# Optimization experiments

Measured on AMD Instinct MI355X. Metric: run time of the kernel, lower is better.

The kernel has to match this reference:

```python
import jax, jax.numpy as jnp
import numpy as np

B_SZ, L, H, P, G, N, CS = 2, 2048, 32, 64, 1, 128, 256


def _i8(k, shape):
    return jax.random.randint(k, shape, -127, 128, dtype=jnp.int32).astype(jnp.int8)


def setup_inputs() -> dict:
    key = jax.random.key(0)
    k = jax.random.split(key, 7)
    return {
        "x": _i8(k[0], (B_SZ, L, H, P)),          # quantized int8 activations
        "dt": _i8(k[1], (B_SZ, L, H)),
        "B": _i8(k[2], (B_SZ, L, G, N)),
        "C": _i8(k[3], (B_SZ, L, G, N)),
        "q_A_log": _i8(k[4], (H,)),               # int8 quantized A_log
        "q_D": _i8(k[5], (H,)),                   # int8 quantized D (D_has_hdim=False)
        "dt_bias": jax.random.normal(k[6], (H,), jnp.float32) * 0.1,
        "A_log_scale": jnp.float32(0.02),
        "D_scale": jnp.float32(0.01),
        "dt_scale": jnp.float32(0.03),
        "x_scale": jnp.float32(0.05),
        "B_scale": jnp.float32(0.05),
        "C_scale": jnp.float32(0.05),
    }


def _chunk_scan(x, dt, B, C, q_A_log, q_D, dt_bias,
                A_log_scale, D_scale, dt_scale, x_scale, B_scale, C_scale):
    f32 = jnp.float32
    b, l, h, p = x.shape
    g, n = B.shape[2], B.shape[3]
    cs = CS
    nc = l // cs

    # --- inline dequantization (per-tensor scales, nhead/ndim groups == 0) ---
    xf = x.astype(f32) * x_scale                       # (b, l, h, p)
    dtf = jax.nn.softplus(dt.astype(f32) * dt_scale + dt_bias)   # (b, l, h), dt_limit=(0, inf)
    A = -jnp.exp(q_A_log.astype(f32) * A_log_scale)    # (h,)
    Bf = B.astype(f32) * B_scale                       # (b, l, g, n)
    Cf = C.astype(f32) * C_scale

    # --- chunk the sequence ---
    xc = xf.reshape(b, nc, cs, h, p)
    dtc = dtf.reshape(b, nc, cs, h)
    Bc = Bf.reshape(b, nc, cs, g, n)
    Cc = Cf.reshape(b, nc, cs, g, n)
    rep = h // g
    Bh = jnp.repeat(Bc, rep, axis=3)                   # (b, nc, cs, h, n)
    Ch = jnp.repeat(Cc, rep, axis=3)

    dA = dtc * A                                       # (b, nc, cs, h), <= 0
    cum = jnp.cumsum(dA, axis=2)                       # cumulative log-decay within chunk

    # --- per-chunk states: sum_s exp(cum[-1]-cum[s]) * dt[s] * B[s] (x) x[s] ---
    decay_states = jnp.exp(cum[:, :, -1:, :] - cum)    # (b, nc, cs, h)
    states = jnp.einsum('bzlhn,bzlh,bzlhp->bzhpn', Bh, dtc * decay_states, xc)

    # --- inter-chunk recurrence (sequential scan over chunks) ---
    chunk_decay = jnp.exp(cum[:, :, -1, :])            # (b, nc, h)

    def step(carry, inp):
        s_c, d_c = inp                                 # (b, h, p, n), (b, h)
        new = d_c[:, :, None, None] * carry + s_c
        return new, carry                              # emit state entering this chunk

    states_t = jnp.moveaxis(states, 1, 0)              # (nc, b, h, p, n)
    decay_t = jnp.moveaxis(chunk_decay, 1, 0)          # (nc, b, h)
    final_state, prev_states = jax.lax.scan(
        step, jnp.zeros((b, h, p, n), f32), (states_t, decay_t))
    prev_states = jnp.moveaxis(prev_states, 0, 1)      # (b, nc, h, p, n)

    # --- inter-chunk output: C[l] . state_in * exp(cum[l]) ---
    y_inter = jnp.einsum('bzlhn,bzhpn,bzlh->bzlhp', Ch, prev_states, jnp.exp(cum))

    # --- intra-chunk output: causal (C.B) attention with decay weights ---
    cumT = jnp.moveaxis(cum, 3, 2)                     # (b, nc, h, cs)
    diff = cumT[..., :, None] - cumT[..., None, :]     # (b, nc, h, cs, cs): cum[l]-cum[s]
    mask = jnp.tril(jnp.ones((cs, cs), bool))
    decay_m = jnp.exp(jnp.where(mask, diff, -jnp.inf)) # zero above diagonal, no overflow
    scores = (jnp.einsum('bzlhn,bzshn->bzhls', Ch, Bh)
              * decay_m
              * jnp.moveaxis(dtc, 3, 2)[..., None, :])
    y_intra = jnp.einsum('bzhls,bzshp->bzlhp', scores, xc)

    # --- skip connection D * x (per-head D) ---
    Df = q_D.astype(f32) * D_scale                     # (h,)
    y = (y_intra + y_inter).reshape(b, l, h, p) + xf * Df[None, None, :, None]
    return y


def reference(x, dt, B, C, q_A_log, q_D, dt_bias,
              A_log_scale, D_scale, dt_scale, x_scale, B_scale, C_scale):
    return _chunk_scan(x, dt, B, C, q_A_log, q_D, dt_bias,
                       A_log_scale, D_scale, dt_scale, x_scale, B_scale, C_scale)
```

## Files before the change

kernel.cpp:

```cpp
#include <hip/hip_runtime.h>
#include <math.h>

#define BB 2
#define LSEQ 2048
#define H 32
#define PDIM 64
#define NDIM 128
#define CS 256
#define NC 8

typedef _Float16 half8 __attribute__((ext_vector_type(8)));
typedef _Float16 half4 __attribute__((ext_vector_type(4)));
typedef float floatx4 __attribute__((ext_vector_type(4)));


__device__ __forceinline__ int dot4i8(int a, int b, int c) {
#if __has_builtin(__builtin_amdgcn_sdot4)
    return __builtin_amdgcn_sdot4(a, b, c, false);
#else
    c += ((a << 24) >> 24) * ((b << 24) >> 24);
    c += ((a << 16) >> 24) * ((b << 16) >> 24);
    c += ((a << 8) >> 24) * ((b << 8) >> 24);
    c += (a >> 24) * (b >> 24);
    return c;
#endif
}

__global__ __launch_bounds__(256) void kA(
    const int* __restrict__ Bm, const int* __restrict__ Cm,
    const float* __restrict__ Bs_p, const float* __restrict__ Cs_p,
    _Float16* __restrict__ CBh, _Float16* __restrict__ Bt16T, _Float16* __restrict__ C16T)
{
    __shared__ int Bi[64][33];
    __shared__ int Ci[64][33];
    int t = threadIdx.x;
    int r = blockIdx.x % 26;
    int zz = blockIdx.x / 26;
    int z = zz & 7, b = zz >> 3;
    int bz = b * NC + z;
    if (r < 10) {
        const int LT[10] = {0,1,1,2,2,2,3,3,3,3};
        const int ST[10] = {0,0,1,0,1,2,0,1,2,3};
        int l0 = LT[r] * 64, s0 = ST[r] * 64;
        const int* Bp = Bm + (size_t)(b * LSEQ + z * CS + s0) * NDIM;
        const int* Cp = Cm + (size_t)(b * LSEQ + z * CS + l0) * NDIM;
        for (int i = t; i < 64 * 32; i += 256) {
            int rr = i >> 5, k = i & 31;
            const int* sb = Bp + rr * NDIM + k * 4;
            const int* sc = Cp + rr * NDIM + k * 4;
            Bi[rr][k] = (sb[0] & 255) | ((sb[1] & 255) << 8) | ((sb[2] & 255) << 16) | ((sb[3] & 255) << 24);
            Ci[rr][k] = (sc[0] & 255) | ((sc[1] & 255) << 8) | ((sc[2] & 255) << 16) | ((sc[3] & 255) << 24);
        }
        __syncthreads();
        float cbscale = (*Bs_p) * (*Cs_p);
        int ll = t & 63, lg = t >> 6;
        int acc[16];
#pragma unroll
        for (int i = 0; i < 16; ++i) acc[i] = 0;
        for (int k = 0; k < 32; ++k) {
            int cw = Ci[ll][k];
#pragma unroll
            for (int si = 0; si < 16; ++si)
                acc[si] = dot4i8(cw, Bi[lg * 16 + si][k], acc[si]);
        }
        int l = l0 + ll;
        int l16 = l >> 4, lm = l & 15;
        int sb8 = (s0 + lg * 16) >> 3;
        _Float16* bp = CBh + ((size_t)(bz * 16 + l16) * 32 + sb8) * 128 + lm * 8;
#pragma unroll
        for (int g = 0; g < 2; ++g) {
            half8 v;
#pragma unroll
            for (int i = 0; i < 8; ++i) v[i] = (_Float16)((float)acc[g * 8 + i] * cbscale);
            *(half8*)(bp + g * 128) = v;
        }
    } else {
        int slice = r - 10;
        {
            int lm = t >> 4, n8 = t & 15;
            const int* cp = Cm + (size_t)(b * LSEQ + z * CS + slice * 16 + lm) * NDIM + n8 * 8;
            int4 c0 = *(const int4*)cp;
            int4 c1 = *(const int4*)(cp + 4);
            half8 v;
            v[0] = (_Float16)(float)c0.x; v[1] = (_Float16)(float)c0.y;
            v[2] = (_Float16)(float)c0.z; v[3] = (_Float16)(float)c0.w;
            v[4] = (_Float16)(float)c1.x; v[5] = (_Float16)(float)c1.y;
            v[6] = (_Float16)(float)c1.z; v[7] = (_Float16)(float)c1.w;
            *(half8*)(C16T + ((size_t)(bz * 16 + slice) * 16 + n8) * 128 + lm * 8) = v;
        }
        {
            int nm = t & 15, s8l = t >> 4;
            int n16 = slice & 7, s8 = (slice >> 3) * 16 + s8l;
            const int* bp = Bm + (size_t)(b * LSEQ + z * CS + s8 * 8) * NDIM + n16 * 16 + nm;
            half8 v;
#pragma unroll
            for (int j = 0; j < 8; ++j) v[j] = (_Float16)(float)bp[(size_t)j * NDIM];
            *(half8*)(Bt16T + ((size_t)(bz * 8 + n16) * 32 + s8) * 128 + nm * 8) = v;
        }
    }
}

#define P16_STRIDE 4360
__global__ __launch_bounds__(256) void k013(
    const int* __restrict__ dt, const int* __restrict__ qA, const float* __restrict__ dt_bias,
    const float* __restrict__ A_scale_p, const float* __restrict__ dt_scale_p,
    const int* __restrict__ xq, const float* __restrict__ xs_p, const float* __restrict__ Bs_p,
    const _Float16* __restrict__ Bt16T,
    float* __restrict__ cum, float* __restrict__ cAg, float* __restrict__ cdecay,
    signed char* __restrict__ x8, _Float16* __restrict__ statesF16)
{
    __shared__ float cumS[CS];
    __shared__ float cB[CS];
    __shared__ float wsum[4];
    __shared__ _Float16 xcS[3 * P16_STRIDE + 31 * 136 + 128];
    int t = threadIdx.x;
    int h = blockIdx.x & 31, z = (blockIdx.x >> 5) & 7, b = blockIdx.x >> 8;
    int bz = b * NC + z, bzh = bz * H + h;
    int lane6 = t & 63, w = t >> 6;

    float A = -__expf((float)qA[h] * (*A_scale_p));
    float raw = (float)dt[(size_t)(b * LSEQ + z * CS + t) * H + h];
    float xin = raw * (*dt_scale_p) + dt_bias[h];
    float sp = (xin > 20.f) ? xin : log1pf(__expf(xin));
    float v = sp * A;
#pragma unroll
    for (int off = 1; off < 64; off <<= 1) {
        float u = __shfl_up(v, off, 64);
        if (lane6 >= off) v += u;
    }
    if (lane6 == 63) wsum[w] = v;
    __syncthreads();
    float add = 0.f;
    for (int wv = 0; wv < w; ++wv) add += wsum[wv];
    float cumv = v + add;
    float cl = wsum[0] + wsum[1] + wsum[2] + wsum[3];
    float xs = *xs_p;
    cum[(size_t)bzh * CS + t] = cumv;
    cAg[(size_t)bzh * CS + t] = sp * xs;
    if (t == 0) cdecay[bzh] = __expf(cl);
    cumS[t] = cumv;
    cB[t] = sp * __expf(cl - cumv) * xs * (*Bs_p);
    __syncthreads();

    int pq = t & 15, srow = t >> 4;
    const int* xb = xq + ((size_t)(b * LSEQ + z * CS) * H + h) * PDIM + pq * 4;
    signed char* x8b = x8 + ((size_t)(b * LSEQ + z * CS) * H + h) * PDIM + pq * 4;
    int p0 = pq * 4;
    int pbase = (p0 >> 4) * P16_STRIDE + ((p0 & 15) * 8);
    for (int j = 0; j < 16; ++j) {
        int s = j * 16 + srow;
        int4 w4 = *(const int4*)(xb + (size_t)s * (H * PDIM));
        float c = cB[s];
        int sbase = pbase + (s >> 3) * 136 + (s & 7);
        signed char pk[4];
        int xi[4] = {w4.x, w4.y, w4.z, w4.w};
#pragma unroll
        for (int pp = 0; pp < 4; ++pp) {
            xcS[sbase + pp * 8] = (_Float16)((float)xi[pp] * c);
            pk[pp] = (signed char)xi[pp];
        }
        *(int*)(x8b + (size_t)s * (H * PDIM)) = *(int*)pk;
    }
    __syncthreads();

    int m = lane6 & 15, q = lane6 >> 4;
    const _Float16* abase = xcS + w * P16_STRIDE + m * 8;
    const _Float16* bbase = Bt16T + (size_t)(bz * 8) * 32 * 128 + m * 8;
    floatx4 acc[8] = {};
    for (int kk = 0; kk < 8; ++kk) {
        if (cl - cumS[kk * 32 + 31] < -30.f) continue;
        int s8k = kk * 4 + q;
        half8 a = *(const half8*)(abase + s8k * 136);
#pragma unroll
        for (int nt = 0; nt < 8; ++nt) {
            half8 bf = *(const half8*)(bbase + ((size_t)nt * 32 + s8k) * 128);
            acc[nt] = __builtin_amdgcn_mfma_f32_16x16x32_f16(a, bf, acc[nt], 0, 0, 0);
        }
    }
    _Float16* sb = statesF16 + (size_t)bzh * 8192;
#pragma unroll
    for (int nt = 0; nt < 8; ++nt)
#pragma unroll
        for (int rr = 0; rr < 4; ++rr)
            sb[(size_t)(w * 16 + nt * 2 + (m >> 3)) * 128 + (q * 4 + rr) * 8 + (m & 7)] =
                (_Float16)(acc[nt][rr] * 0.0625f);
}

__global__ __launch_bounds__(256) void k4_scan(
    const float* __restrict__ cdecay, const _Float16* __restrict__ statesF16,
    _Float16* __restrict__ statesHT)
{
    int idx = blockIdx.x * 256 + threadIdx.x;
    int off4 = (idx & 2047) * 4;
    int h = (idx >> 11) & 31, b = idx >> 16;
    floatx4 carry = {};
    for (int z = 0; z < NC; ++z) {
        int bzh = (b * NC + z) * H + h;
        half4 v4 = *(const half4*)(statesF16 + (size_t)bzh * 8192 + off4);
        float d = cdecay[bzh];
        half4 o;
#pragma unroll
        for (int i = 0; i < 4; ++i) o[i] = (_Float16)carry[i];
        *(half4*)(statesHT + (size_t)bzh * 8192 + off4) = o;
#pragma unroll
        for (int i = 0; i < 4; ++i) carry[i] = d * carry[i] + (float)v4[i];
    }
}

#define XT_PITCH 136
__global__ __launch_bounds__(256) void k56(
    const signed char* __restrict__ x8, const int* __restrict__ qD,
    const float* __restrict__ cum, const float* __restrict__ cAg,
    const _Float16* __restrict__ CBh, const _Float16* __restrict__ C16T,
    const _Float16* __restrict__ statesHT,
    const float* __restrict__ Cs_p, const float* __restrict__ xs_p, const float* __restrict__ Ds_p,
    float* __restrict__ out)
{
    __shared__ float cumL[CS];
    __shared__ __align__(16) char smem[4 * 32 * XT_PITCH * 2];
    _Float16* xT = (_Float16*)smem;
    float (*ep)[65] = (float(*)[65])smem;
    int t = threadIdx.x;
    int h = blockIdx.x & 31, z = (blockIdx.x >> 5) & 7, b = blockIdx.x >> 8;
    int bz = b * NC + z, bzh = bz * H + h;
    cumL[t] = cum[(size_t)bzh * CS + t];
    float cav = cAg[(size_t)bzh * CS + t];

    {
        const signed char* xrow = x8 + ((size_t)(b * LSEQ + z * CS + t) * H + h) * PDIM;
        int s8 = t >> 3, sj = t & 7;
        int4 r4 = *(const int4*)xrow;
        int4 r5 = *(const int4*)(xrow + 16);
        int4 r6 = *(const int4*)(xrow + 32);
        int4 r7 = *(const int4*)(xrow + 48);
        int words[16] = {r4.x, r4.y, r4.z, r4.w, r5.x, r5.y, r5.z, r5.w,
                         r6.x, r6.y, r6.z, r6.w, r7.x, r7.y, r7.z, r7.w};
#pragma unroll
        for (int wi = 0; wi < 16; ++wi) {
            int wv = words[wi];
#pragma unroll
            for (int bi = 0; bi < 4; ++bi) {
                int p = wi * 4 + bi;
                int val = (wv << (24 - 8 * bi)) >> 24;
                xT[((p >> 4) * 32 + s8) * XT_PITCH + (p & 15) * 8 + sj] =
                    (_Float16)((float)val * cav);
            }
        }
    }
    __syncthreads();

    int w = t >> 6, lane = t & 63, m = lane & 15, q = lane >> 4;
    floatx4 acc[4][4] = {};

    const _Float16* shb = statesHT + (size_t)bzh * 8192 + m * 8;
    const _Float16* cbase = C16T + (size_t)bz * 16 * 16 * 128 + m * 8;
    bool interact[4];
#pragma unroll
    for (int j = 0; j < 4; ++j) interact[j] = (cumL[(4 * j + w) * 16] > -80.f);
    for (int kk = 0; kk < 4; ++kk) {
        int n8 = kk * 4 + q;
        half8 bf[4];
#pragma unroll
        for (int pt = 0; pt < 4; ++pt)
            bf[pt] = *(const half8*)(shb + (pt * 16 + n8) * 128);
#pragma unroll
        for (int j = 0; j < 4; ++j) {
            if (!interact[j]) continue;
            half8 ha = *(const half8*)(cbase + ((size_t)(4 * j + w) * 16 + n8) * 128);
#pragma unroll
            for (int pt = 0; pt < 4; ++pt)
                acc[j][pt] = __builtin_amdgcn_mfma_f32_16x16x32_f16(ha, bf[pt], acc[j][pt], 0, 0, 0);
        }
    }
    float Cs16 = (*Cs_p) * 16.0f;
#pragma unroll
    for (int j = 0; j < 4; ++j)
#pragma unroll
        for (int r = 0; r < 4; ++r) {
            float e = __expf(cumL[(4 * j + w) * 16 + q * 4 + r]) * Cs16;
#pragma unroll
            for (int pt = 0; pt < 4; ++pt) acc[j][pt][r] *= e;
        }

    const _Float16* cbtb = CBh + (size_t)bz * 16 * 32 * 128 + m * 8;
    for (int kk = 0; kk < 8; ++kk) {
        int jmin = (2 * kk - w + 3) >> 2;
        if (jmin < 0) jmin = 0;
        if (jmin > 3) continue;
        int s8 = kk * 4 + q;
        half8 bf[4];
#pragma unroll
        for (int pt = 0; pt < 4; ++pt)
            bf[pt] = *(const half8*)(xT + (size_t)(pt * 32 + s8) * XT_PITCH + m * 8);
#pragma unroll
        for (int j = 0; j < 4; ++j) {
            if (j < jmin) continue;
            int l16 = 4 * j + w;
            if (cumL[l16 * 16] - cumL[kk * 32 + 31] < -30.f) continue;
            int lA = l16 * 16 + m;
            float cum_l = cumL[lA];
            half8 cb8 = *(const half8*)(cbtb + ((size_t)l16 * 32 + s8) * 128);
            half8 a;
#pragma unroll
            for (int jj = 0; jj < 8; ++jj) {
                int s = kk * 32 + q * 8 + jj;
                float wv = (float)cb8[jj] * __expf(cum_l - cumL[s]);
                a[jj] = (_Float16)((s <= lA) ? wv : 0.f);
            }
#pragma unroll
            for (int pt = 0; pt < 4; ++pt)
                acc[j][pt] = __builtin_amdgcn_mfma_f32_16x16x32_f16(a, bf[pt], acc[j][pt], 0, 0, 0);
        }
    }

    float xsDf = (*xs_p) * ((float)qD[h] * (*Ds_p));
    __syncthreads();
#pragma unroll
    for (int pass = 0; pass < 2; ++pass) {
#pragma unroll
        for (int jj = 0; jj < 2; ++jj) {
            int j = pass * 2 + jj;
            int lbase = (((4 * j + w) * 16) & 127) + q * 4;
#pragma unroll
            for (int r = 0; r < 4; ++r)
#pragma unroll
                for (int pt = 0; pt < 4; ++pt)
                    ep[lbase + r][pt * 16 + m] = acc[j][pt][r];
        }
        __syncthreads();
        int lloc = t >> 1;
        int l = pass * 128 + lloc;
        size_t go = ((size_t)(b * LSEQ + z * CS + l) * H + h) * PDIM + (t & 1) * 32;
        const float* er = &ep[lloc][(t & 1) * 32];
        const signed char* xp8 = x8 + go;
#pragma unroll
        for (int it = 0; it < 8; ++it) {
            int xw = *(const int*)(xp8 + it * 4);
            floatx4 vv;
            vv[0] = er[it * 4 + 0] + (float)((xw << 24) >> 24) * xsDf;
            vv[1] = er[it * 4 + 1] + (float)((xw << 16) >> 24) * xsDf;
            vv[2] = er[it * 4 + 2] + (float)((xw << 8) >> 24) * xsDf;
            vv[3] = er[it * 4 + 3] + (float)(xw >> 24) * xsDf;
            *(floatx4*)(out + go + it * 4) = vv;
        }
        __syncthreads();
    }
}

extern "C" void kernel_launch(void* const* d_in, const int* in_sizes, int n_in,
                              void* d_out, int out_size, void* d_ws, size_t ws_size,
                              hipStream_t stream)
{
    const int* xq = (const int*)d_in[0];
    const int* dt = (const int*)d_in[1];
    const int* Bm = (const int*)d_in[2];
    const int* Cm = (const int*)d_in[3];
    const int* qA = (const int*)d_in[4];
    const int* qD = (const int*)d_in[5];
    const float* dt_bias = (const float*)d_in[6];
    const float* A_scale = (const float*)d_in[7];
    const float* D_scale = (const float*)d_in[8];
    const float* dt_scale = (const float*)d_in[9];
    const float* x_scale = (const float*)d_in[10];
    const float* B_scale = (const float*)d_in[11];
    const float* C_scale = (const float*)d_in[12];
    float* out = (float*)d_out;

    char* ws = (char*)d_ws;
    float* cum           = (float*)(ws);
    float* cAg           = (float*)(ws + 524288);
    float* cdecay        = (float*)(ws + 1048576);
    _Float16* CBh        = (_Float16*)(ws + 1050624);
    _Float16* statesF16  = (_Float16*)(ws + 3147776);
    _Float16* statesHT   = (_Float16*)(ws + 11536384);
    _Float16* Bt16T      = (_Float16*)(ws + 19924992);
    _Float16* C16T       = (_Float16*)(ws + 20973568);
    signed char* x8      = (signed char*)(ws + 22022144);

    kA<<<dim3(416), dim3(256), 0, stream>>>(Bm, Cm, B_scale, C_scale, CBh, Bt16T, C16T);
    k013<<<dim3(512), dim3(256), 0, stream>>>(dt, qA, dt_bias, A_scale, dt_scale,
                                              xq, x_scale, B_scale, Bt16T,
                                              cum, cAg, cdecay, x8, statesF16);
    k4_scan<<<dim3(512), dim3(256), 0, stream>>>(cdecay, statesF16, statesHT);
    k56<<<dim3(512), dim3(256), 0, stream>>>(x8, qD, cum, cAg, CBh, C16T, statesHT,
                                             C_scale, x_scale, D_scale, out);
}
```

Before: 157.4 us.

## Split state and output kernels across two blocks per chunk-head for more parallelism

k013 and k56 now launch 1024 blocks instead of 512. Each chunk-head pair is split in two: by P-dimension halves in the state kernel and by interleaved L-row groups in the output kernel. Per-block LDS and accumulators shrink, and launch bounds request 4 blocks per SM, which should raise occupancy on the 256-CU device. The cost is duplicated cumsum/softplus work and duplicated xT staging in both halves. A small cumL vector-load change in the intra-chunk loop is also included.

```diff
diff --git a/kernel.cpp b/kernel.cpp
--- a/kernel.cpp
+++ b/kernel.cpp
@@ -101,7 +101,7 @@
 }
 
 #define P16_STRIDE 4360
-__global__ __launch_bounds__(256) void k013(
+__global__ __launch_bounds__(256, 4) void k013(
     const int* __restrict__ dt, const int* __restrict__ qA, const float* __restrict__ dt_bias,
     const float* __restrict__ A_scale_p, const float* __restrict__ dt_scale_p,
     const int* __restrict__ xq, const float* __restrict__ xs_p, const float* __restrict__ Bs_p,
@@ -112,9 +112,11 @@
     __shared__ float cumS[CS];
     __shared__ float cB[CS];
     __shared__ float wsum[4];
-    __shared__ _Float16 xcS[3 * P16_STRIDE + 31 * 136 + 128];
+    __shared__ _Float16 xcS[P16_STRIDE + 31 * 136 + 136];
     int t = threadIdx.x;
-    int h = blockIdx.x & 31, z = (blockIdx.x >> 5) & 7, b = blockIdx.x >> 8;
+    int half = blockIdx.x & 1;
+    int id = blockIdx.x >> 1;
+    int h = id & 31, z = (id >> 5) & 7, b = id >> 8;
     int bz = b * NC + z, bzh = bz * H + h;
     int lane6 = t & 63, w = t >> 6;
 
@@ -135,20 +137,23 @@
     float cumv = v + add;
     float cl = wsum[0] + wsum[1] + wsum[2] + wsum[3];
     float xs = *xs_p;
-    cum[(size_t)bzh * CS + t] = cumv;
-    cAg[(size_t)bzh * CS + t] = sp * xs;
-    if (t == 0) cdecay[bzh] = __expf(cl);
+    if (half == 0) {
+        cum[(size_t)bzh * CS + t] = cumv;
+        cAg[(size_t)bzh * CS + t] = sp * xs;
+        if (t == 0) cdecay[bzh] = __expf(cl);
+    }
     cumS[t] = cumv;
     cB[t] = sp * __expf(cl - cumv) * xs * (*Bs_p);
     __syncthreads();
 
-    int pq = t & 15, srow = t >> 4;
-    const int* xb = xq + ((size_t)(b * LSEQ + z * CS) * H + h) * PDIM + pq * 4;
-    signed char* x8b = x8 + ((size_t)(b * LSEQ + z * CS) * H + h) * PDIM + pq * 4;
-    int p0 = pq * 4;
-    int pbase = (p0 >> 4) * P16_STRIDE + ((p0 & 15) * 8);
-    for (int j = 0; j < 16; ++j) {
-        int s = j * 16 + srow;
+    int pq = t & 7, srow = t >> 3;
+    int p0 = half * 32 + pq * 4;
+    const int* xb = xq + ((size_t)(b * LSEQ + z * CS) * H + h) * PDIM + p0;
+    signed char* x8b = x8 + ((size_t)(b * LSEQ + z * CS) * H + h) * PDIM + p0;
+    int plocal = pq * 4;
+    int pbase = (plocal >> 4) * P16_STRIDE + ((plocal & 15) * 8);
+    for (int j = 0; j < 8; ++j) {
+        int s = j * 32 + srow;
         int4 w4 = *(const int4*)(xb + (size_t)s * (H * PDIM));
         float c = cB[s];
         int sbase = pbase + (s >> 3) * 136 + (s & 7);
@@ -164,25 +169,27 @@
     __syncthreads();
 
     int m = lane6 & 15, q = lane6 >> 4;
-    const _Float16* abase = xcS + w * P16_STRIDE + m * 8;
+    int p16l = w & 1, ntb = (w >> 1) * 4;
+    const _Float16* abase = xcS + p16l * P16_STRIDE + m * 8;
     const _Float16* bbase = Bt16T + (size_t)(bz * 8) * 32 * 128 + m * 8;
-    floatx4 acc[8] = {};
+    floatx4 acc[4] = {};
     for (int kk = 0; kk < 8; ++kk) {
         if (cl - cumS[kk * 32 + 31] < -30.f) continue;
         int s8k = kk * 4 + q;
         half8 a = *(const half8*)(abase + s8k * 136);
 #pragma unroll
-        for (int nt = 0; nt < 8; ++nt) {
-            half8 bf = *(const half8*)(bbase + ((size_t)nt * 32 + s8k) * 128);
+        for (int nt = 0; nt < 4; ++nt) {
+            half8 bf = *(const half8*)(bbase + ((size_t)(ntb + nt) * 32 + s8k) * 128);
             acc[nt] = __builtin_amdgcn_mfma_f32_16x16x32_f16(a, bf, acc[nt], 0, 0, 0);
         }
     }
+    int p16g = half * 2 + p16l;
     _Float16* sb = statesF16 + (size_t)bzh * 8192;
 #pragma unroll
-    for (int nt = 0; nt < 8; ++nt)
+    for (int nt = 0; nt < 4; ++nt)
 #pragma unroll
         for (int rr = 0; rr < 4; ++rr)
-            sb[(size_t)(w * 16 + nt * 2 + (m >> 3)) * 128 + (q * 4 + rr) * 8 + (m & 7)] =
+            sb[(size_t)(p16g * 16 + (ntb + nt) * 2 + (m >> 3)) * 128 + (q * 4 + rr) * 8 + (m & 7)] =
                 (_Float16)(acc[nt][rr] * 0.0625f);
 }
 
@@ -208,7 +215,7 @@
 }
 
 #define XT_PITCH 136
-__global__ __launch_bounds__(256) void k56(
+__global__ __launch_bounds__(256, 4) void k56(
     const signed char* __restrict__ x8, const int* __restrict__ qD,
     const float* __restrict__ cum, const float* __restrict__ cAg,
     const _Float16* __restrict__ CBh, const _Float16* __restrict__ C16T,
@@ -221,7 +228,9 @@
     _Float16* xT = (_Float16*)smem;
     float (*ep)[65] = (float(*)[65])smem;
     int t = threadIdx.x;
-    int h = blockIdx.x & 31, z = (blockIdx.x >> 5) & 7, b = blockIdx.x >> 8;
+    int par = blockIdx.x & 1;
+    int id = blockIdx.x >> 1;
+    int h = id & 31, z = (id >> 5) & 7, b = id >> 8;
     int bz = b * NC + z, bzh = bz * H + h;
     cumL[t] = cum[(size_t)bzh * CS + t];
     float cav = cAg[(size_t)bzh * CS + t];
@@ -250,13 +259,13 @@
     __syncthreads();
 
     int w = t >> 6, lane = t & 63, m = lane & 15, q = lane >> 4;
-    floatx4 acc[4][4] = {};
+    floatx4 acc[2][4] = {};
 
     const _Float16* shb = statesHT + (size_t)bzh * 8192 + m * 8;
     const _Float16* cbase = C16T + (size_t)bz * 16 * 16 * 128 + m * 8;
-    bool interact[4];
-#pragma unroll
-    for (int j = 0; j < 4; ++j) interact[j] = (cumL[(4 * j + w) * 16] > -80.f);
+    bool interact[2];
+#pragma unroll
+    for (int jl = 0; jl < 2; ++jl) interact[jl] = (cumL[(4 * par + 8 * jl + w) * 16] > -80.f);
     for (int kk = 0; kk < 4; ++kk) {
         int n8 = kk * 4 + q;
         half8 bf[4];
@@ -264,38 +273,40 @@
         for (int pt = 0; pt < 4; ++pt)
             bf[pt] = *(const half8*)(shb + (pt * 16 + n8) * 128);
 #pragma unroll
-        for (int j = 0; j < 4; ++j) {
-            if (!interact[j]) continue;
-            half8 ha = *(const half8*)(cbase + ((size_t)(4 * j + w) * 16 + n8) * 128);
+        for (int jl = 0; jl < 2; ++jl) {
+            if (!interact[jl]) continue;
+            int l16 = 4 * par + 8 * jl + w;
+            half8 ha = *(const half8*)(cbase + ((size_t)l16 * 16 + n8) * 128);
 #pragma unroll
             for (int pt = 0; pt < 4; ++pt)
-                acc[j][pt] = __builtin_amdgcn_mfma_f32_16x16x32_f16(ha, bf[pt], acc[j][pt], 0, 0, 0);
+                acc[jl][pt] = __builtin_amdgcn_mfma_f32_16x16x32_f16(ha, bf[pt], acc[jl][pt], 0, 0, 0);
         }
     }
     float Cs16 = (*Cs_p) * 16.0f;
 #pragma unroll
-    for (int j = 0; j < 4; ++j)
+    for (int jl = 0; jl < 2; ++jl)
 #pragma unroll
         for (int r = 0; r < 4; ++r) {
-            float e = __expf(cumL[(4 * j + w) * 16 + q * 4 + r]) * Cs16;
-#pragma unroll
-            for (int pt = 0; pt < 4; ++pt) acc[j][pt][r] *= e;
+            float e = __expf(cumL[(4 * par + 8 * jl + w) * 16 + q * 4 + r]) * Cs16;
+#pragma unroll
+            for (int pt = 0; pt < 4; ++pt) acc[jl][pt][r] *= e;
         }
 
     const _Float16* cbtb = CBh + (size_t)bz * 16 * 32 * 128 + m * 8;
+    int l16max = 4 * par + 8 + w;
     for (int kk = 0; kk < 8; ++kk) {
-        int jmin = (2 * kk - w + 3) >> 2;
-        if (jmin < 0) jmin = 0;
-        if (jmin > 3) continue;
+        if (l16max < 2 * kk) continue;
         int s8 = kk * 4 + q;
         half8 bf[4];
 #pragma unroll
         for (int pt = 0; pt < 4; ++pt)
             bf[pt] = *(const half8*)(xT + (size_t)(pt * 32 + s8) * XT_PITCH + m * 8);
-#pragma unroll
-        for (int j = 0; j < 4; ++j) {
-            if (j < jmin) continue;
-            int l16 = 4 * j + w;
+        floatx4 c0 = *(const floatx4*)(&cumL[kk * 32 + q * 8]);
+        floatx4 c1 = *(const floatx4*)(&cumL[kk * 32 + q * 8 + 4]);
+#pragma unroll
+        for (int jl = 0; jl < 2; ++jl) {
+            int l16 = 4 * par + 8 * jl + w;
+            if (l16 < 2 * kk) continue;
             if (cumL[l16 * 16] - cumL[kk * 32 + 31] < -30.f) continue;
             int lA = l16 * 16 + m;
             float cum_l = cumL[lA];
@@ -304,32 +315,32 @@
 #pragma unroll
             for (int jj = 0; jj < 8; ++jj) {
                 int s = kk * 32 + q * 8 + jj;
-                float wv = (float)cb8[jj] * __expf(cum_l - cumL[s]);
+                float cls = (jj < 4) ? c0[jj] : c1[jj - 4];
+                float wv = (float)cb8[jj] * __expf(cum_l - cls);
                 a[jj] = (_Float16)((s <= lA) ? wv : 0.f);
             }
 #pragma unroll
             for (int pt = 0; pt < 4; ++pt)
-                acc[j][pt] = __builtin_amdgcn_mfma_f32_16x16x32_f16(a, bf[pt], acc[j][pt], 0, 0, 0);
+                acc[jl][pt] = __builtin_amdgcn_mfma_f32_16x16x32_f16(a, bf[pt], acc[jl][pt], 0, 0, 0);
         }
     }
 
     float xsDf = (*xs_p) * ((float)qD[h] * (*Ds_p));
     __syncthreads();
 #pragma unroll
-    for (int pass = 0; pass < 2; ++pass) {
-#pragma unroll
-        for (int jj = 0; jj < 2; ++jj) {
-            int j = pass * 2 + jj;
-            int lbase = (((4 * j + w) * 16) & 127) + q * 4;
-#pragma unroll
-            for (int r = 0; r < 4; ++r)
-#pragma unroll
-                for (int pt = 0; pt < 4; ++pt)
-                    ep[lbase + r][pt * 16 + m] = acc[j][pt][r];
-        }
-        __syncthreads();
+    for (int jl = 0; jl < 2; ++jl) {
+        int lbase = jl * 64 + w * 16 + q * 4;
+#pragma unroll
+        for (int r = 0; r < 4; ++r)
+#pragma unroll
+            for (int pt = 0; pt < 4; ++pt)
+                ep[lbase + r][pt * 16 + m] = acc[jl][pt][r];
+    }
+    __syncthreads();
+    {
         int lloc = t >> 1;
-        int l = pass * 128 + lloc;
+        int jl = lloc >> 6, wv = (lloc >> 4) & 3, lm = lloc & 15;
+        int l = (4 * par + 8 * jl + wv) * 16 + lm;
         size_t go = ((size_t)(b * LSEQ + z * CS + l) * H + h) * PDIM + (t & 1) * 32;
         const float* er = &ep[lloc][(t & 1) * 32];
         const signed char* xp8 = x8 + go;
@@ -343,7 +354,6 @@
             vv[3] = er[it * 4 + 3] + (float)(xw >> 24) * xsDf;
             *(floatx4*)(out + go + it * 4) = vv;
         }
-        __syncthreads();
     }
 }
 
@@ -378,10 +388,10 @@
     signed char* x8      = (signed char*)(ws + 22022144);
 
     kA<<<dim3(416), dim3(256), 0, stream>>>(Bm, Cm, B_scale, C_scale, CBh, Bt16T, C16T);
-    k013<<<dim3(512), dim3(256), 0, stream>>>(dt, qA, dt_bias, A_scale, dt_scale,
-                                              xq, x_scale, B_scale, Bt16T,
-                                              cum, cAg, cdecay, x8, statesF16);
+    k013<<<dim3(1024), dim3(256), 0, stream>>>(dt, qA, dt_bias, A_scale, dt_scale,
+                                               xq, x_scale, B_scale, Bt16T,
+                                               cum, cAg, cdecay, x8, statesF16);
     k4_scan<<<dim3(512), dim3(256), 0, stream>>>(cdecay, statesF16, statesHT);
-    k56<<<dim3(512), dim3(256), 0, stream>>>(x8, qD, cum, cAg, CBh, C16T, statesHT,
-                                             C_scale, x_scale, D_scale, out);
-}
+    k56<<<dim3(1024), dim3(256), 0, stream>>>(x8, qD, cum, cAg, CBh, C16T, statesHT,
+                                              C_scale, x_scale, D_scale, out);
+}
```

Result: no change. 156.1 us (-0.8%).
